# Optimization experiments

Measured on AMD Instinct MI355X. Metric: run time of the kernel, lower is better.

The kernel has to match this reference:

```python
import jax, jax.numpy as jnp
import numpy as np

DIM = 512
HEADS = 8
DIM_HEAD = 64
INNER = HEADS * DIM_HEAD  # 512
SCALE = DIM_HEAD ** -0.5
LN_EPS = 1e-5


def setup_inputs() -> dict:
    key = jax.random.key(0)
    k1, k2, k3, k4 = jax.random.split(key, 4)
    b, p, n = 4, 64, 256
    x = jax.random.normal(k1, (b, p, n, DIM), dtype=jnp.float32)
    ln_g = jnp.ones((DIM,), jnp.float32)
    ln_b = jnp.zeros((DIM,), jnp.float32)
    # stored as [in, out] for x @ W
    w_qkv = jax.random.normal(k2, (DIM, 3 * INNER), jnp.float32) * (DIM ** -0.5)
    w_out = jax.random.normal(k3, (INNER, DIM), jnp.float32) * (INNER ** -0.5)
    b_out = jnp.zeros((DIM,), jnp.float32)
    return {"x": x, "ln_g": ln_g, "ln_b": ln_b, "w_qkv": w_qkv,
            "w_out": w_out, "b_out": b_out}


def reference(x, ln_g, ln_b, w_qkv, w_out, b_out):
    b, p, n, _ = x.shape
    # LayerNorm over last dim
    mu = jnp.mean(x, axis=-1, keepdims=True)
    var = jnp.mean(jnp.square(x - mu), axis=-1, keepdims=True)
    xn = (x - mu) * jax.lax.rsqrt(var + LN_EPS) * ln_g + ln_b
    # QKV projection (no bias)
    qkv = xn @ w_qkv                                   # [b,p,n,3*INNER]
    q, k, v = jnp.split(qkv, 3, axis=-1)
    def to_heads(t):
        return t.reshape(b, p, n, HEADS, DIM_HEAD).transpose(0, 1, 3, 2, 4)
    q, k, v = to_heads(q), to_heads(k), to_heads(v)    # [b,p,h,n,d]
    dots = jnp.einsum('bphnd,bphmd->bphnm', q, k) * SCALE
    attn = jax.nn.softmax(dots, axis=-1)
    out = jnp.einsum('bphnm,bphmd->bphnd', attn, v)    # [b,p,h,n,d]
    out = out.transpose(0, 1, 3, 2, 4).reshape(b, p, n, INNER)
    return out @ w_out + b_out
```

## Files before the change

### kernel.cpp

```cpp
#include <hip/hip_runtime.h>
#include <stdint.h>

#define DIMD 512
#define HEADS 8
#define DHEAD 64
#define NSEQ 256
#define NGRP 256
#define TRIPLE 1536
#define ATT_SCALE 0.125f

typedef float f32x4 __attribute__((ext_vector_type(4)));
typedef _Float16 half8 __attribute__((ext_vector_type(8)));
typedef _Float16 half4 __attribute__((ext_vector_type(4)));

#define GLD16(gp, lp) __builtin_amdgcn_global_load_lds( \
    (const __attribute__((address_space(1))) void*)(gp), \
    (__attribute__((address_space(3))) void*)(lp), 16, 0, 0)
#define BAR() __builtin_amdgcn_s_barrier()
#define VMW(n) asm volatile("s_waitcnt vmcnt(" #n ")" ::: "memory")

__global__ __launch_bounds__(256) void k_pre(const float* __restrict__ x,
                                             const float* __restrict__ g,
                                             const float* __restrict__ b,
                                             const float* __restrict__ wq,
                                             const float* __restrict__ wo,
                                             _Float16* __restrict__ xn,
                                             _Float16* __restrict__ wtq,
                                             _Float16* __restrict__ wto) {
  int bid = blockIdx.x;
  if (bid < 4096) {
    int id = bid * 256 + threadIdx.x;
    if (id < DIMD * TRIPLE) {
      int k = id / TRIPLE, n = id % TRIPLE;
      wtq[n * DIMD + k] = (_Float16)wq[id];
    } else {
      int j = id - DIMD * TRIPLE;
      int k = j / DIMD, n = j % DIMD;
      wto[n * DIMD + k] = (_Float16)wo[j];
    }
    return;
  }
  int row = (bid - 4096) * 4 + (threadIdx.x >> 6);
  int lane = threadIdx.x & 63;
  const float* xr = x + (size_t)row * DIMD + lane * 8;
  float v[8];
  *(f32x4*)(v)     = *(const f32x4*)(xr);
  *(f32x4*)(v + 4) = *(const f32x4*)(xr + 4);
  float s = 0.f, ss = 0.f;
#pragma unroll
  for (int j = 0; j < 8; ++j) { s += v[j]; ss += v[j] * v[j]; }
#pragma unroll
  for (int m = 1; m < 64; m <<= 1) { s += __shfl_xor(s, m); ss += __shfl_xor(ss, m); }
  float mean = s * (1.f / DIMD);
  float var  = ss * (1.f / DIMD) - mean * mean;
  float rstd = rsqrtf(var + 1e-5f);
  const float* gp = g + lane * 8;
  const float* bp = b + lane * 8;
  half8 o;
#pragma unroll
  for (int j = 0; j < 8; ++j) o[j] = (_Float16)((v[j] - mean) * rstd * gp[j] + bp[j]);
  *(half8*)(xn + (size_t)row * DIMD + lane * 8) = o;
}

template <int N, int LDA, bool F32OUT>
__global__ __launch_bounds__(512, 2) void k_gemm8(const _Float16* __restrict__ A,
                                                  const _Float16* __restrict__ BT,
                                                  _Float16* __restrict__ Ch,
                                                  float* __restrict__ Cf,
                                                  const float* __restrict__ bias) {
  constexpr int NT = N / 256;
  constexpr int NWG = 256 * NT;
  constexpr int CPX = NWG / 8;
  int b = blockIdx.x;
  int logical = (b & 7) * CPX + (b >> 3);
  int mt = logical / NT, nt = logical % NT;
  int m0 = mt * 256, n0 = nt * 256;

  int tid = threadIdx.x, lane = tid & 63, w = tid >> 6;
  int wrow = w >> 2, wcol = w & 3;
  int l15 = lane & 15, lg = lane >> 4;
  const int sr = lane >> 3;
  const int ss = lane & 7;

  __shared__ _Float16 S[65536];

  f32x4 acc[8][4] = {};
  half8 af[4][2], bf0[2][2], bf1[2][2];

  auto stageA = [&](int d, int kt, int hf) {
#pragma unroll
    for (int cc = 0; cc < 2; ++cc) {
      int rbase = cc * 128 + hf * 64 + w * 8;
      const _Float16* gp = A + (size_t)(m0 + rbase + sr) * LDA + kt * 64 + (ss ^ sr) * 8;
      _Float16* l = &S[d * 32768 + rbase * 64];
      GLD16(gp, l);
    }
  };
  auto stageB = [&](int d, int kt, int hf) {
#pragma unroll
    for (int cc = 0; cc < 2; ++cc) {
      int i = cc * 64 + w * 8;
      int rbase = (i >> 5) * 64 + hf * 32 + (i & 31);
      const _Float16* gp = BT + (size_t)(n0 + rbase + sr) * 512 + kt * 64 + (ss ^ sr) * 8;
      _Float16* l = &S[d * 32768 + 16384 + rbase * 64];
      GLD16(gp, l);
    }
  };
  auto loadA = [&](int c, int mh) {
#pragma unroll
    for (int mf = 0; mf < 4; ++mf) {
      int row = wrow * 128 + mh * 64 + mf * 16 + l15;
#pragma unroll
      for (int kk = 0; kk < 2; ++kk) {
        int byte = row * 128 + ((kk * 64 + lg * 16) ^ ((row & 7) << 4));
        af[mf][kk] = *(const half8*)((const char*)&S[c * 32768] + byte);
      }
    }
  };
  auto loadB = [&](int c, int nh, half8 (&bf)[2][2]) {
#pragma unroll
    for (int nf = 0; nf < 2; ++nf) {
      int row = wcol * 64 + nh * 32 + nf * 16 + l15;
#pragma unroll
      for (int kk = 0; kk < 2; ++kk) {
        int byte = row * 128 + ((kk * 64 + lg * 16) ^ ((row & 7) << 4));
        bf[nf][kk] = *(const half8*)((const char*)&S[c * 32768 + 16384] + byte);
      }
    }
  };
  auto quad = [&](int mh, int nh, half8 (&bf)[2][2]) {
    __builtin_amdgcn_s_setprio(1);
#pragma unroll
    for (int mf = 0; mf < 4; ++mf)
#pragma unroll
      for (int nf = 0; nf < 2; ++nf)
#pragma unroll
        for (int kk = 0; kk < 2; ++kk)
          acc[mh * 4 + mf][nh * 2 + nf] = __builtin_amdgcn_mfma_f32_16x16x32_f16(
              af[mf][kk], bf[nf][kk], acc[mh * 4 + mf][nh * 2 + nf], 0, 0, 0);
    __builtin_amdgcn_s_setprio(0);
  };

  stageA(0, 0, 0); stageB(0, 0, 0); stageB(0, 0, 1); stageA(0, 0, 1);
  VMW(4); BAR();

  for (int t = 0; t < 7; ++t) {
    int c = t & 1, d = c ^ 1;
    loadA(c, 0); loadB(c, 0, bf0);
    stageA(d, t + 1, 0);
    BAR(); quad(0, 0, bf0); VMW(4); BAR();
    loadB(c, 1, bf1);
    stageB(d, t + 1, 0);
    BAR(); quad(0, 1, bf1); VMW(4); BAR();
    loadA(c, 1);
    stageB(d, t + 1, 1);
    BAR(); quad(1, 0, bf0); BAR();
    stageA(d, t + 1, 1);
    BAR(); quad(1, 1, bf1); VMW(4); BAR();
  }
  {
    loadA(1, 0); loadB(1, 0, bf0);
    BAR(); quad(0, 0, bf0); VMW(2); BAR();
    loadB(1, 1, bf1);
    BAR(); quad(0, 1, bf1); VMW(0); BAR();
    loadA(1, 1);
    BAR(); quad(1, 0, bf0); BAR();
    BAR(); quad(1, 1, bf1); BAR();
  }

  float bb[4];
  if constexpr (F32OUT) {
#pragma unroll
    for (int nq = 0; nq < 4; ++nq)
      bb[nq] = bias[n0 + wcol * 64 + (nq >> 1) * 32 + (nq & 1) * 16 + l15];
  }
#pragma unroll
  for (int mq = 0; mq < 8; ++mq)
#pragma unroll
    for (int nq = 0; nq < 4; ++nq)
#pragma unroll
      for (int r = 0; r < 4; ++r) {
        int row = m0 + wrow * 128 + (mq >> 2) * 64 + (mq & 3) * 16 + lg * 4 + r;
        int col = n0 + wcol * 64 + (nq >> 1) * 32 + (nq & 1) * 16 + l15;
        if constexpr (F32OUT)
          Cf[(size_t)row * N + col] = acc[mq][nq][r] + bb[nq];
        else
          Ch[(size_t)row * N + col] = (_Float16)acc[mq][nq][r];
      }
}

__global__ __launch_bounds__(256, 2) void k_attn(_Float16* __restrict__ qkv) {
  int g = blockIdx.x >> 3, h = blockIdx.x & 7;
  int tid = threadIdx.x, lane = tid & 63, w = tid >> 6;
  int l15 = lane & 15, lg = lane >> 4;
  __shared__ _Float16 Kt[64 * 64];
  __shared__ _Float16 Vt[64 * 72];
  __shared__ _Float16 Pl[4][64 * 72];
  const size_t base = (size_t)g * NSEQ * TRIPLE;

  half8 qf[4][2];
#pragma unroll
  for (int nq = 0; nq < 4; ++nq)
#pragma unroll
    for (int kd = 0; kd < 2; ++kd)
      qf[nq][kd] = *(const half8*)&qkv[base + (size_t)(w * 64 + nq * 16 + l15) * TRIPLE
                                       + h * 64 + kd * 32 + lg * 8];

  f32x4 oacc[4][4] = {};
  float mrun[4], lrun[4];
#pragma unroll
  for (int nq = 0; nq < 4; ++nq) { mrun[nq] = -3.0e38f; lrun[nq] = 0.f; }

  const int srow = lane >> 3;
  const int sslot = lane & 7;

  for (int kt = 0; kt < 4; ++kt) {
    __syncthreads();
#pragma unroll
    for (int rnd = 0; rnd < 2; ++rnd) {
      int rbase = rnd * 32 + w * 8;
      const _Float16* gp = &qkv[base + (size_t)(kt * 64 + rbase + srow) * TRIPLE
                                + 512 + h * 64 + (sslot ^ srow) * 8];
      GLD16(gp, &Kt[rbase * 64]);
    }
#pragma unroll
    for (int i = 0; i < 2; ++i) {
      int idx = tid + i * 256;
      int key = idx >> 3, dh0 = (idx & 7) * 8;
      half8 vv = *(const half8*)&qkv[base + (size_t)(kt * 64 + key) * TRIPLE + 1024 + h * 64 + dh0];
#pragma unroll
      for (int j = 0; j < 8; ++j) Vt[(dh0 + j) * 72 + key] = vv[j];
    }
    VMW(0);
    __syncthreads();

    f32x4 st[4][4] = {};
#pragma unroll
    for (int kd = 0; kd < 2; ++kd) {
      half8 kf[4];
#pragma unroll
      for (int mk = 0; mk < 4; ++mk) {
        int r = mk * 16 + l15;
        int byte = r * 128 + ((kd * 64 + lg * 16) ^ ((r & 7) << 4));
        kf[mk] = *(const half8*)((const char*)Kt + byte);
      }
#pragma unroll
      for (int mk = 0; mk < 4; ++mk)
#pragma unroll
        for (int nq = 0; nq < 4; ++nq)
          st[mk][nq] = __builtin_amdgcn_mfma_f32_16x16x32_f16(kf[mk], qf[nq][kd], st[mk][nq], 0, 0, 0);
    }

    float alpha[4];
#pragma unroll
    for (int nq = 0; nq < 4; ++nq) {
      float pm = -3.0e38f;
#pragma unroll
      for (int mk = 0; mk < 4; ++mk)
#pragma unroll
        for (int r = 0; r < 4; ++r) {
          st[mk][nq][r] *= ATT_SCALE;
          pm = fmaxf(pm, st[mk][nq][r]);
        }
      pm = fmaxf(pm, __shfl_xor(pm, 16));
      pm = fmaxf(pm, __shfl_xor(pm, 32));
      float mn = fmaxf(mrun[nq], pm);
      alpha[nq] = __expf(mrun[nq] - mn);
      mrun[nq] = mn;
      float ps = 0.f;
#pragma unroll
      for (int mk = 0; mk < 4; ++mk) {
        half4 p4;
#pragma unroll
        for (int r = 0; r < 4; ++r) {
          float e = __expf(st[mk][nq][r] - mn);
          ps += e;
          p4[r] = (_Float16)e;
        }
        *(half4*)&Pl[w][(nq * 16 + l15) * 72 + mk * 16 + lg * 4] = p4;
      }
      ps += __shfl_xor(ps, 16);
      ps += __shfl_xor(ps, 32);
      lrun[nq] = lrun[nq] * alpha[nq] + ps;
    }

#pragma unroll
    for (int mp = 0; mp < 4; ++mp)
#pragma unroll
      for (int r = 0; r < 4; ++r) {
        float av = __shfl(alpha[mp], lg * 4 + r);
#pragma unroll
        for (int nd = 0; nd < 4; ++nd) oacc[mp][nd][r] *= av;
      }

    __syncthreads();

#pragma unroll
    for (int kp = 0; kp < 2; ++kp) {
      int co = kp * 32 + lg * 8;
      half8 pf[4], vf[4];
#pragma unroll
      for (int mp = 0; mp < 4; ++mp) pf[mp] = *(const half8*)&Pl[w][(mp * 16 + l15) * 72 + co];
#pragma unroll
      for (int nd = 0; nd < 4; ++nd) vf[nd] = *(const half8*)&Vt[(nd * 16 + l15) * 72 + co];
#pragma unroll
      for (int mp = 0; mp < 4; ++mp)
#pragma unroll
        for (int nd = 0; nd < 4; ++nd)
          oacc[mp][nd] = __builtin_amdgcn_mfma_f32_16x16x32_f16(pf[mp], vf[nd], oacc[mp][nd], 0, 0, 0);
    }
  }

#pragma unroll
  for (int mp = 0; mp < 4; ++mp)
#pragma unroll
    for (int r = 0; r < 4; ++r) {
      float li = 1.f / __shfl(lrun[mp], lg * 4 + r);
      int q = w * 64 + mp * 16 + lg * 4 + r;
#pragma unroll
      for (int nd = 0; nd < 4; ++nd)
        qkv[base + (size_t)q * TRIPLE + h * 64 + nd * 16 + l15] =
            (_Float16)(oacc[mp][nd][r] * li);
    }
}

extern "C" void kernel_launch(void* const* d_in, const int* in_sizes, int n_in,
                              void* d_out, int out_size, void* d_ws, size_t ws_size,
                              hipStream_t stream) {
  const float* x     = (const float*)d_in[0];
  const float* ln_g  = (const float*)d_in[1];
  const float* ln_b  = (const float*)d_in[2];
  const float* w_qkv = (const float*)d_in[3];
  const float* w_out = (const float*)d_in[4];
  const float* b_out = (const float*)d_in[5];

  char* ws = (char*)d_ws;
  _Float16* qkv = (_Float16*)ws;
  _Float16* wtq = (_Float16*)(ws + 201326592ull);
  _Float16* wto = (_Float16*)(ws + 201326592ull + 1572864ull);
  _Float16* xn  = (_Float16*)d_out;
  float* out    = (float*)d_out;

  k_pre<<<20480, 256, 0, stream>>>(x, ln_g, ln_b, w_qkv, w_out, xn, wtq, wto);
  k_gemm8<TRIPLE, DIMD, false><<<1536, 512, 0, stream>>>(xn, wtq, qkv, nullptr, nullptr);
  k_attn<<<2048, 256, 0, stream>>>(qkv);
  k_gemm8<DIMD, TRIPLE, true><<<512, 512, 0, stream>>>(qkv, wto, nullptr, out, b_out);
}
```

Baseline: 288.2 us.

## Software-pipeline GEMM main loop and tile weight transpose through shared memory

The GEMM main loop is restructured so the last MFMA quadrant of each k-step is deferred into the next iteration, with a second A-fragment register set (af0/af1). This lets LDS fragment loads overlap MFMA work and drops several barriers per iteration. Separately, the weight transpose/convert in the preprocessing kernel now goes through a 64x64 shared-memory tile, giving coalesced reads and writes instead of strided scattered stores, and its block count drops from 4096 to 256. The extra fragment registers raise register pressure, which could reduce occupancy at two workgroups per CU.

```diff
diff --git a/kernel.cpp b/kernel.cpp
--- a/kernel.cpp
+++ b/kernel.cpp
@@ -28,19 +28,30 @@
                                              _Float16* __restrict__ wtq,
                                              _Float16* __restrict__ wto) {
   int bid = blockIdx.x;
-  if (bid < 4096) {
-    int id = bid * 256 + threadIdx.x;
-    if (id < DIMD * TRIPLE) {
-      int k = id / TRIPLE, n = id % TRIPLE;
-      wtq[n * DIMD + k] = (_Float16)wq[id];
-    } else {
-      int j = id - DIMD * TRIPLE;
-      int k = j / DIMD, n = j % DIMD;
-      wto[n * DIMD + k] = (_Float16)wo[j];
+  if (bid < 256) {
+    __shared__ float T[64][65];
+    const float* src; _Float16* dst; int spitch, ti, tj;
+    if (bid < 192) { src = wq; dst = wtq; spitch = TRIPLE; ti = bid / 24; tj = bid % 24; }
+    else { int t = bid - 192; src = wo; dst = wto; spitch = DIMD; ti = t >> 3; tj = t & 7; }
+#pragma unroll
+    for (int it = 0; it < 4; ++it) {
+      int idx = it * 256 + threadIdx.x;
+      int rr = idx >> 4, c4 = (idx & 15) * 4;
+      *(f32x4*)&T[rr][c4] = *(const f32x4*)&src[(size_t)(ti * 64 + rr) * spitch + tj * 64 + c4];
+    }
+    __syncthreads();
+#pragma unroll
+    for (int it = 0; it < 2; ++it) {
+      int idx = it * 256 + threadIdx.x;
+      int rr2 = idx >> 3, c8 = (idx & 7) * 8;
+      half8 o;
+#pragma unroll
+      for (int j = 0; j < 8; ++j) o[j] = (_Float16)T[c8 + j][rr2];
+      *(half8*)&dst[(size_t)(tj * 64 + rr2) * DIMD + ti * 64 + c8] = o;
     }
     return;
   }
-  int row = (bid - 4096) * 4 + (threadIdx.x >> 6);
+  int row = (bid - 256) * 4 + (threadIdx.x >> 6);
   int lane = threadIdx.x & 63;
   const float* xr = x + (size_t)row * DIMD + lane * 8;
   float v[8];
@@ -71,8 +82,8 @@
   constexpr int NT = N / 256;
   constexpr int NWG = 256 * NT;
   constexpr int CPX = NWG / 8;
-  int b = blockIdx.x;
-  int logical = (b & 7) * CPX + (b >> 3);
+  int bb_ = blockIdx.x;
+  int logical = (bb_ & 7) * CPX + (bb_ >> 3);
   int mt = logical / NT, nt = logical % NT;
   int m0 = mt * 256, n0 = nt * 256;
 
@@ -85,15 +96,14 @@
   __shared__ _Float16 S[65536];
 
   f32x4 acc[8][4] = {};
-  half8 af[4][2], bf0[2][2], bf1[2][2];
+  half8 af0[4][2], af1[4][2], bf0[2][2], bf1[2][2];
 
   auto stageA = [&](int d, int kt, int hf) {
 #pragma unroll
     for (int cc = 0; cc < 2; ++cc) {
       int rbase = cc * 128 + hf * 64 + w * 8;
       const _Float16* gp = A + (size_t)(m0 + rbase + sr) * LDA + kt * 64 + (ss ^ sr) * 8;
-      _Float16* l = &S[d * 32768 + rbase * 64];
-      GLD16(gp, l);
+      GLD16(gp, &S[d * 32768 + rbase * 64]);
     }
   };
   auto stageB = [&](int d, int kt, int hf) {
@@ -102,11 +112,10 @@
       int i = cc * 64 + w * 8;
       int rbase = (i >> 5) * 64 + hf * 32 + (i & 31);
       const _Float16* gp = BT + (size_t)(n0 + rbase + sr) * 512 + kt * 64 + (ss ^ sr) * 8;
-      _Float16* l = &S[d * 32768 + 16384 + rbase * 64];
-      GLD16(gp, l);
-    }
-  };
-  auto loadA = [&](int c, int mh) {
+      GLD16(gp, &S[d * 32768 + 16384 + rbase * 64]);
+    }
+  };
+  auto loadA = [&](int c, int mh, half8 (&af)[4][2]) {
 #pragma unroll
     for (int mf = 0; mf < 4; ++mf) {
       int row = wrow * 128 + mh * 64 + mf * 16 + l15;
@@ -128,7 +137,7 @@
       }
     }
   };
-  auto quad = [&](int mh, int nh, half8 (&bf)[2][2]) {
+  auto quad = [&](int mh, int nh, half8 (&af)[4][2], half8 (&bf)[2][2]) {
     __builtin_amdgcn_s_setprio(1);
 #pragma unroll
     for (int mf = 0; mf < 4; ++mf)
@@ -144,35 +153,32 @@
   stageA(0, 0, 0); stageB(0, 0, 0); stageB(0, 0, 1); stageA(0, 0, 1);
   VMW(4); BAR();
 
-  for (int t = 0; t < 7; ++t) {
-    int c = t & 1, d = c ^ 1;
-    loadA(c, 0); loadB(c, 0, bf0);
-    stageA(d, t + 1, 0);
-    BAR(); quad(0, 0, bf0); VMW(4); BAR();
+#pragma unroll
+  for (int t = 0; t < 8; ++t) {
+    const int c = t & 1, d = c ^ 1;
+    loadA(c, 0, af0); loadB(c, 0, bf0);
+    if (t > 0) quad(1, 1, af1, bf1);
+    if (t < 7) { stageA(d, t + 1, 0); VMW(4); } else { VMW(2); }
+    BAR();
     loadB(c, 1, bf1);
-    stageB(d, t + 1, 0);
-    BAR(); quad(0, 1, bf1); VMW(4); BAR();
-    loadA(c, 1);
-    stageB(d, t + 1, 1);
-    BAR(); quad(1, 0, bf0); BAR();
-    stageA(d, t + 1, 1);
-    BAR(); quad(1, 1, bf1); VMW(4); BAR();
+    quad(0, 0, af0, bf0);
+    if (t < 7) { stageB(d, t + 1, 0); VMW(4); } else { VMW(0); }
+    BAR();
+    loadA(c, 1, af1);
+    quad(0, 1, af0, bf1);
+    if (t < 7) stageB(d, t + 1, 1);
+    BAR();
+    quad(1, 0, af1, bf0);
+    if (t < 7) { stageA(d, t + 1, 1); VMW(4); }
+    BAR();
   }
-  {
-    loadA(1, 0); loadB(1, 0, bf0);
-    BAR(); quad(0, 0, bf0); VMW(2); BAR();
-    loadB(1, 1, bf1);
-    BAR(); quad(0, 1, bf1); VMW(0); BAR();
-    loadA(1, 1);
-    BAR(); quad(1, 0, bf0); BAR();
-    BAR(); quad(1, 1, bf1); BAR();
-  }
-
-  float bb[4];
+  quad(1, 1, af1, bf1);
+
+  float bbv[4];
   if constexpr (F32OUT) {
 #pragma unroll
     for (int nq = 0; nq < 4; ++nq)
-      bb[nq] = bias[n0 + wcol * 64 + (nq >> 1) * 32 + (nq & 1) * 16 + l15];
+      bbv[nq] = bias[n0 + wcol * 64 + (nq >> 1) * 32 + (nq & 1) * 16 + l15];
   }
 #pragma unroll
   for (int mq = 0; mq < 8; ++mq)
@@ -183,7 +189,7 @@
         int row = m0 + wrow * 128 + (mq >> 2) * 64 + (mq & 3) * 16 + lg * 4 + r;
         int col = n0 + wcol * 64 + (nq >> 1) * 32 + (nq & 1) * 16 + l15;
         if constexpr (F32OUT)
-          Cf[(size_t)row * N + col] = acc[mq][nq][r] + bb[nq];
+          Cf[(size_t)row * N + col] = acc[mq][nq][r] + bbv[nq];
         else
           Ch[(size_t)row * N + col] = (_Float16)acc[mq][nq][r];
       }
@@ -341,7 +347,7 @@
   _Float16* xn  = (_Float16*)d_out;
   float* out    = (float*)d_out;
 
-  k_pre<<<20480, 256, 0, stream>>>(x, ln_g, ln_b, w_qkv, w_out, xn, wtq, wto);
+  k_pre<<<16640, 256, 0, stream>>>(x, ln_g, ln_b, w_qkv, w_out, xn, wtq, wto);
   k_gemm8<TRIPLE, DIMD, false><<<1536, 512, 0, stream>>>(xn, wtq, qkv, nullptr, nullptr);
   k_attn<<<2048, 256, 0, stream>>>(qkv);
   k_gemm8<DIMD, TRIPLE, true><<<512, 512, 0, stream>>>(qkv, wto, nullptr, out, b_out);
```

New measurement: 278.8 us. 1.03x faster.
